# Optimization experiments

Measured on AMD Instinct MI355X. Metric: run time of the kernel, lower is better.

Reference implementation:

```python
import jax, jax.numpy as jnp
import numpy as np

N_NODES = 4096
IN_FEAT = 256
N_HEADS = 8
N_HIDDEN = 64  # out_features // n_heads
NEG_SLOPE = 0.2
EDGE_PROB = 0.05


def setup_inputs() -> dict:
    key = jax.random.key(0)
    k1, k2, k3, k4 = jax.random.split(key, 4)
    h = jax.random.normal(k1, (N_NODES, IN_FEAT), dtype=jnp.float32)
    # binary adjacency mask [N, N, 1] (broadcast over heads), as in the torch asserts
    adj_mat = (jax.random.uniform(k2, (N_NODES, N_NODES, 1)) < EDGE_PROB).astype(jnp.float32)
    # nn.Linear(in_features, n_heads*n_hidden, bias=False) weight: [H*F, in]
    W = jax.random.normal(k3, (N_HEADS * N_HIDDEN, IN_FEAT), dtype=jnp.float32) / np.sqrt(IN_FEAT)
    # nn.Linear(2*n_hidden, 1, bias=False) weight, flattened: [2*F]
    a = jax.random.normal(k4, (2 * N_HIDDEN,), dtype=jnp.float32) / np.sqrt(2 * N_HIDDEN)
    return {"h": h, "adj_mat": adj_mat, "W": W, "a": a}


def reference(h, adj_mat, W, a):
    n = h.shape[0]
    # g: [N, H, F]
    g = (h @ W.T).reshape(n, N_HEADS, N_HIDDEN)
    # attn(cat[g_i, g_j]) == a_l . g_i + a_r . g_j  (linear, no bias)
    a_l = a[:N_HIDDEN]
    a_r = a[N_HIDDEN:]
    el = jnp.einsum('ihf,f->ih', g, a_l)  # [N, H]
    er = jnp.einsum('jhf,f->jh', g, a_r)  # [N, H]
    e = jax.nn.leaky_relu(el[:, None, :] + er[None, :, :], NEG_SLOPE)  # [N, N, H]
    # note: original multiplies scores by adjacency (not masked_fill)
    e = e * adj_mat  # adj broadcasts over heads
    att = jax.nn.softmax(e, axis=1)  # softmax over source nodes j
    # dropout is identity at eval (dropout_rate=0.0)
    out = jnp.einsum('ijh,jhf->ihf', att, g)  # [N, H, F]
    return out.reshape(n, N_HEADS * N_HIDDEN)
```

## Files before the change

kernel.cpp:

```cpp
#include <hip/hip_runtime.h>

#define N_NODES 4096
#define IN_FEAT 256
#define N_HEADS 8
#define N_HIDDEN 64
#define OUT_FEAT (N_HEADS * N_HIDDEN)
#define NEG_SLOPE 0.2f

typedef _Float16 half8 __attribute__((ext_vector_type(8)));
typedef _Float16 h2 __attribute__((ext_vector_type(2)));
typedef float floatx4 __attribute__((ext_vector_type(4)));
typedef float f4 __attribute__((ext_vector_type(4)));

__global__ __launch_bounds__(256) void produce(
    const float* __restrict__ H, const float* __restrict__ adj,
    const float* __restrict__ Wt, const float* __restrict__ a,
    _Float16* __restrict__ GT16, float* __restrict__ elT,
    _Float16* __restrict__ eR1h, _Float16* __restrict__ eR2h,
    unsigned long long* __restrict__ bits) {
  __shared__ _Float16 SM[4 * 64 * 64];
  const int t = threadIdx.x;
  const int bx = blockIdx.x, by = blockIdx.y;

  if (by >= 8) {
    const int c = bx * 8 + (by - 8);
    const size_t W0 = (size_t)c * 512;
    const int wv = t >> 6, lane = t & 63;
    for (int k0 = 0; k0 < 128; k0 += 8) {
      float v[8];
#pragma unroll
      for (int k = 0; k < 8; ++k)
        v[k] = adj[(W0 + wv * 128 + k0 + k) * 64 + lane];
#pragma unroll
      for (int k = 0; k < 8; ++k) {
        unsigned long long m = __ballot(v[k] != 0.f);
        if (lane == 0) bits[W0 + wv * 128 + k0 + k] = m;
      }
    }
    return;
  }

  _Float16* Ah = SM;
  _Float16* Al = SM + 4096;
  _Float16* Bh = SM + 8192;
  _Float16* Bl = SM + 12288;
  const int w = t >> 6, l = t & 63;
  const int n16 = l & 15, q = l >> 4;
  const int bi = bx, bo = by;
  const int m0 = bi * 64 + w * 16;

  floatx4 acc[4];
#pragma unroll
  for (int ct = 0; ct < 4; ++ct) acc[ct] = (floatx4)0.f;

  for (int kc = 0; kc < 4; ++kc) {
    if (kc) __syncthreads();
#pragma unroll
    for (int p = 0; p < 4; ++p) {
      const int idx = p * 256 + t;
      const int r = idx >> 4;
      const int c4 = (idx & 15) << 2;
      const int dst = r * 64 + ((((idx & 15) >> 1)) ^ (r & 7)) * 8 + (idx & 1) * 4;
      float4 hv = *(const float4*)(H + (size_t)(bi * 64 + r) * IN_FEAT + kc * 64 + c4);
      float4 wv = *(const float4*)(Wt + (size_t)(bo * 64 + r) * IN_FEAT + kc * 64 + c4);
      union { _Float16 h[4]; int2 d; } hh_, hl_, wh_, wl_;
      hh_.h[0] = (_Float16)hv.x; hh_.h[1] = (_Float16)hv.y;
      hh_.h[2] = (_Float16)hv.z; hh_.h[3] = (_Float16)hv.w;
      hl_.h[0] = (_Float16)(hv.x - (float)hh_.h[0]);
      hl_.h[1] = (_Float16)(hv.y - (float)hh_.h[1]);
      hl_.h[2] = (_Float16)(hv.z - (float)hh_.h[2]);
      hl_.h[3] = (_Float16)(hv.w - (float)hh_.h[3]);
      wh_.h[0] = (_Float16)wv.x; wh_.h[1] = (_Float16)wv.y;
      wh_.h[2] = (_Float16)wv.z; wh_.h[3] = (_Float16)wv.w;
      wl_.h[0] = (_Float16)(wv.x - (float)wh_.h[0]);
      wl_.h[1] = (_Float16)(wv.y - (float)wh_.h[1]);
      wl_.h[2] = (_Float16)(wv.z - (float)wh_.h[2]);
      wl_.h[3] = (_Float16)(wv.w - (float)wh_.h[3]);
      *(int2*)&Ah[dst] = hh_.d;
      *(int2*)&Al[dst] = hl_.d;
      *(int2*)&Bh[dst] = wh_.d;
      *(int2*)&Bl[dst] = wl_.d;
    }
    __syncthreads();
#pragma unroll
    for (int ks = 0; ks < 2; ++ks) {
      const int ao = (w * 16 + n16) * 64 + (((ks << 2) + q) ^ (n16 & 7)) * 8;
      half8 Afh = *(const half8*)&Ah[ao];
      half8 Afl = *(const half8*)&Al[ao];
#pragma unroll
      for (int ct = 0; ct < 4; ++ct) {
        const int bofs = (ct * 16 + n16) * 64 + (((ks << 2) + q) ^ (n16 & 7)) * 8;
        half8 Bfh = *(const half8*)&Bh[bofs];
        half8 Bfl = *(const half8*)&Bl[bofs];
        acc[ct] = __builtin_amdgcn_mfma_f32_16x16x32_f16(Afh, Bfh, acc[ct], 0, 0, 0);
        acc[ct] = __builtin_amdgcn_mfma_f32_16x16x32_f16(Afl, Bfh, acc[ct], 0, 0, 0);
        acc[ct] = __builtin_amdgcn_mfma_f32_16x16x32_f16(Afh, Bfl, acc[ct], 0, 0, 0);
      }
    }
  }

  float aLv[4], aRv[4];
#pragma unroll
  for (int ct = 0; ct < 4; ++ct) {
    aLv[ct] = a[ct * 16 + n16];
    aRv[ct] = a[64 + ct * 16 + n16];
  }
#pragma unroll
  for (int reg = 0; reg < 4; ++reg) {
    float sl = 0.f, sr = 0.f;
#pragma unroll
    for (int ct = 0; ct < 4; ++ct) {
      sl = fmaf(acc[ct][reg], aLv[ct], sl);
      sr = fmaf(acc[ct][reg], aRv[ct], sr);
    }
#pragma unroll
    for (int off = 1; off < 16; off <<= 1) {
      sl += __shfl_xor(sl, off);
      sr += __shfl_xor(sr, off);
    }
    if (n16 == 0) {
      const int rowi = m0 + q * 4 + reg;
      elT[(size_t)bo * N_NODES + rowi] = sl;
      eR1h[(size_t)bo * N_NODES + rowi] = (_Float16)__expf(sr);
      eR2h[(size_t)bo * N_NODES + rowi] = (_Float16)__expf(0.2f * sr);
    }
  }

  __syncthreads();
  _Float16* LG = SM;
#pragma unroll
  for (int ct = 0; ct < 4; ++ct)
#pragma unroll
    for (int reg = 0; reg < 4; ++reg)
      LG[(w * 16 + q * 4 + reg) * 72 + ct * 16 + n16] = (_Float16)acc[ct][reg];
  __syncthreads();
  {
    const int f = t >> 2, jq = t & 3;
    union { _Float16 hh[16]; int4 v[2]; } u;
#pragma unroll
    for (int k = 0; k < 16; ++k) u.hh[k] = LG[(jq * 16 + k) * 72 + f];
    _Float16* dst = GT16 + (size_t)(bo * 64 + f) * N_NODES + bi * 64 + jq * 16;
    *(int4*)dst = u.v[0];
    *(int4*)(dst + 8) = u.v[1];
  }
}

__global__ __launch_bounds__(256) void attn_v12(
    const unsigned long long* __restrict__ bits, const _Float16* __restrict__ GT16,
    const float* __restrict__ elT, const _Float16* __restrict__ eR1h,
    const _Float16* __restrict__ eR2h, float* __restrict__ out) {
  __shared__ __align__(16) _Float16 Gt[2][2][2048];
  __shared__ __align__(16) _Float16 eRs1[2][2][32];
  __shared__ __align__(16) _Float16 eRs2[2][2][32];
  __shared__ float eL1s[32], eL2s[32];
  __shared__ float Zh1[32], Zfull[32];

  const int t = threadIdx.x;
  const int ib = blockIdx.x, h = blockIdx.y;
  const int i0 = ib * 32;
  const int w = t >> 6, l = t & 63, n16 = l & 15, q = l >> 4;
  const int rt = w & 1, jh = w >> 1;

  const _Float16* gsrcs[2];
  int ldsbase[2];
#pragma unroll
  for (int c = 0; c < 2; ++c) {
    const int flat = c * 256 + t;
    const int fjh = flat >> 8;
    const int ff = (flat >> 2) & 63;
    const int ss = flat & 3;
    const int cg = ss ^ ((ff >> 1) & 3);
    gsrcs[c] = GT16 + (size_t)(h * 64 + ff) * N_NODES + fjh * 2048 + cg * 8;
    ldsbase[c] = (c * 256 + w * 64) * 8;
  }
  const int era = t >> 3, ejh = (t >> 2) & 1, eseg = t & 3;
  const _Float16* esrc0 = (era ? eR2h : eR1h) + (size_t)h * N_NODES + ejh * 2048 + eseg * 8;
  const unsigned* bp = (const unsigned*)bits + (size_t)(i0 + rt * 16 + n16) * 128 + jh * 64;

  if (t < 32) {
    float e = elT[(size_t)h * N_NODES + i0 + t];
    eL1s[t] = __expf(e);
    eL2s[t] = __expf(0.2f * e);
  }
#pragma unroll
  for (int c = 0; c < 2; ++c)
    __builtin_amdgcn_global_load_lds(
        (const __attribute__((address_space(1))) unsigned int*)gsrcs[c],
        (__attribute__((address_space(3))) unsigned int*)(&Gt[0][0][0] + ldsbase[c]),
        16, 0, 0);
  if (t < 16) {
    int4 ev = *(const int4*)esrc0;
    *(int4*)&(era ? eRs2 : eRs1)[0][ejh][eseg * 8] = ev;
  }
  unsigned bvc = bp[0];
  __syncthreads();

  const _Float16 e1f = (_Float16)eL1s[rt * 16 + n16];
  const _Float16 e2f = (_Float16)eL2s[rt * 16 + n16];
  const h2 eL1h2 = {e1f, e1f};
  const h2 eL2h2 = {e2f, e2f};
  half8 Bones;
#pragma unroll
  for (int k = 0; k < 8; ++k) Bones[k] = (n16 == 0) ? (_Float16)1.f : (_Float16)0.f;

  floatx4 acc[4];
#pragma unroll
  for (int ft = 0; ft < 4; ++ft) acc[ft] = (floatx4)0.f;
  floatx4 acc5 = (floatx4)0.f;

  int par = 0;
  for (int step = 0; step < 64; ++step) {
    int4 ev;
    unsigned bvn = bvc;
    if (step + 1 < 64) {
      const int np = par ^ 1;
#pragma unroll
      for (int c = 0; c < 2; ++c)
        __builtin_amdgcn_global_load_lds(
            (const __attribute__((address_space(1))) unsigned int*)(gsrcs[c] + (step + 1) * 32),
            (__attribute__((address_space(3))) unsigned int*)(&Gt[np][0][0] + ldsbase[c]),
            16, 0, 0);
      if (t < 16) ev = *(const int4*)(esrc0 + (step + 1) * 32);
      bvn = bp[step + 1];
    }
    const _Float16* gt = &Gt[par][jh][0];
    {
      const unsigned byte = (bvc >> (q * 8)) & 0xffu;
      uint4 r1 = *(const uint4*)&eRs1[par][jh][q * 8];
      uint4 r2 = *(const uint4*)&eRs2[par][jh][q * 8];
      const unsigned r1a[4] = {r1.x, r1.y, r1.z, r1.w};
      const unsigned r2a[4] = {r2.x, r2.y, r2.z, r2.w};
      unsigned pr[4];
#pragma unroll
      for (int kk = 0; kk < 4; ++kk) {
        h2 pa = eL1h2 * __builtin_bit_cast(h2, r1a[kk]);
        h2 pb = eL2h2 * __builtin_bit_cast(h2, r2a[kk]);
        h2 pv = __builtin_elementwise_max(pa, pb);
        unsigned y = (byte >> (2 * kk)) & 3u;
        unsigned b01 = (y | (y << 15)) & 0x00010001u;
        unsigned keep = b01 * 0xffffu;
        pr[kk] = (__builtin_bit_cast(unsigned, pv) & keep) | (0x3C003C00u & ~keep);
      }
      const uint4 prv = {pr[0], pr[1], pr[2], pr[3]};
      half8 Af = __builtin_bit_cast(half8, prv);
#pragma unroll
      for (int ft = 0; ft < 4; ++ft) {
        half8 Bf = *(const half8*)&gt[(ft * 16 + n16) * 32 + ((q ^ ((n16 >> 1) & 3))) * 8];
        acc[ft] = __builtin_amdgcn_mfma_f32_16x16x32_f16(Af, Bf, acc[ft], 0, 0, 0);
      }
      acc5 = __builtin_amdgcn_mfma_f32_16x16x32_f16(Af, Bones, acc5, 0, 0, 0);
    }
    if (step + 1 < 64 && t < 16)
      *(int4*)&(era ? eRs2 : eRs1)[par ^ 1][ejh][eseg * 8] = ev;
    bvc = bvn;
    __syncthreads();
    par ^= 1;
  }

  float* comb = (float*)&Gt[0][0][0];
  if (jh == 1) {
#pragma unroll
    for (int ft = 0; ft < 4; ++ft)
#pragma unroll
      for (int reg = 0; reg < 4; ++reg)
        comb[(rt * 16 + q * 4 + reg) * 68 + ft * 16 + n16] = acc[ft][reg];
    if (n16 == 0) {
#pragma unroll
      for (int reg = 0; reg < 4; ++reg) Zh1[rt * 16 + q * 4 + reg] = acc5[reg];
    }
  }
  __syncthreads();
  if (jh == 0) {
#pragma unroll
    for (int ft = 0; ft < 4; ++ft)
#pragma unroll
      for (int reg = 0; reg < 4; ++reg)
        acc[ft][reg] += comb[(rt * 16 + q * 4 + reg) * 68 + ft * 16 + n16];
    if (n16 == 0) {
#pragma unroll
      for (int reg = 0; reg < 4; ++reg) {
        const int row = rt * 16 + q * 4 + reg;
        Zfull[row] = acc5[reg] + Zh1[row];
      }
    }
  }
  __syncthreads();
  if (jh == 0) {
#pragma unroll
    for (int reg = 0; reg < 4; ++reg) {
      const int row = rt * 16 + q * 4 + reg;
      const float invz = 1.f / Zfull[row];
      float* op = out + (size_t)(i0 + row) * OUT_FEAT + h * 64;
#pragma unroll
      for (int ft = 0; ft < 4; ++ft) op[ft * 16 + n16] = acc[ft][reg] * invz;
    }
  }
}

extern "C" void kernel_launch(void* const* d_in, const int* in_sizes, int n_in,
                              void* d_out, int out_size, void* d_ws, size_t ws_size,
                              hipStream_t stream) {
  const float* h   = (const float*)d_in[0];
  const float* adj = (const float*)d_in[1];
  const float* W   = (const float*)d_in[2];
  const float* a   = (const float*)d_in[3];
  float* out = (float*)d_out;

  char* ws = (char*)d_ws;
  _Float16* GT16 = (_Float16*)ws;
  unsigned long long* bits = (unsigned long long*)(ws + 4u * 1024 * 1024);
  float* elT = (float*)(ws + 6u * 1024 * 1024);
  _Float16* eR1h = (_Float16*)(ws + 6u * 1024 * 1024 + 128 * 1024);
  _Float16* eR2h = (_Float16*)(ws + 6u * 1024 * 1024 + 192 * 1024);

  produce<<<dim3(64, 16), 256, 0, stream>>>(h, adj, W, a, GT16, elT, eR1h, eR2h, bits);
  attn_v12<<<dim3(128, 8), 256, 0, stream>>>(bits, GT16, elT, eR1h, eR2h, out);
}
```

Baseline: 171.2 us.

## Split attention source dimension across two blocks and add combine kernel

Splits the attention kernel's loop over source nodes into two halves along a new grid z dimension, doubling the grid from 1024 to 2048 blocks, each doing 32 steps instead of 64. Partial numerators go to out or a workspace buffer, and partial normalizers go to Zp. A new combine kernel sums the halves and divides by Z. This targets low occupancy on a 256-CU device at the cost of an extra launch and extra global traffic for the partial outputs. It also raises launch bounds to hint at 8 blocks per CU.

```diff
diff --git a/kernel.cpp b/kernel.cpp
--- a/kernel.cpp
+++ b/kernel.cpp
@@ -145,10 +145,11 @@
   }
 }
 
-__global__ __launch_bounds__(256) void attn_v12(
+__global__ __launch_bounds__(256, 8) void attn_v13(
     const unsigned long long* __restrict__ bits, const _Float16* __restrict__ GT16,
     const float* __restrict__ elT, const _Float16* __restrict__ eR1h,
-    const _Float16* __restrict__ eR2h, float* __restrict__ out) {
+    const _Float16* __restrict__ eR2h, float* __restrict__ out,
+    float* __restrict__ O1, float* __restrict__ Zp) {
   __shared__ __align__(16) _Float16 Gt[2][2][2048];
   __shared__ __align__(16) _Float16 eRs1[2][2][32];
   __shared__ __align__(16) _Float16 eRs2[2][2][32];
@@ -156,7 +157,7 @@
   __shared__ float Zh1[32], Zfull[32];
 
   const int t = threadIdx.x;
-  const int ib = blockIdx.x, h = blockIdx.y;
+  const int ib = blockIdx.x, h = blockIdx.y, jz = blockIdx.z;
   const int i0 = ib * 32;
   const int w = t >> 6, l = t & 63, n16 = l & 15, q = l >> 4;
   const int rt = w & 1, jh = w >> 1;
@@ -170,12 +171,14 @@
     const int ff = (flat >> 2) & 63;
     const int ss = flat & 3;
     const int cg = ss ^ ((ff >> 1) & 3);
-    gsrcs[c] = GT16 + (size_t)(h * 64 + ff) * N_NODES + fjh * 2048 + cg * 8;
+    gsrcs[c] = GT16 + (size_t)(h * 64 + ff) * N_NODES + jz * 2048 + fjh * 1024 + cg * 8;
     ldsbase[c] = (c * 256 + w * 64) * 8;
   }
   const int era = t >> 3, ejh = (t >> 2) & 1, eseg = t & 3;
-  const _Float16* esrc0 = (era ? eR2h : eR1h) + (size_t)h * N_NODES + ejh * 2048 + eseg * 8;
-  const unsigned* bp = (const unsigned*)bits + (size_t)(i0 + rt * 16 + n16) * 128 + jh * 64;
+  const _Float16* esrc0 =
+      (era ? eR2h : eR1h) + (size_t)h * N_NODES + jz * 2048 + ejh * 1024 + eseg * 8;
+  const unsigned* bp =
+      (const unsigned*)bits + (size_t)(i0 + rt * 16 + n16) * 128 + jz * 64 + jh * 32;
 
   if (t < 32) {
     float e = elT[(size_t)h * N_NODES + i0 + t];
@@ -209,10 +212,10 @@
   floatx4 acc5 = (floatx4)0.f;
 
   int par = 0;
-  for (int step = 0; step < 64; ++step) {
+  for (int step = 0; step < 32; ++step) {
     int4 ev;
     unsigned bvn = bvc;
-    if (step + 1 < 64) {
+    if (step + 1 < 32) {
       const int np = par ^ 1;
 #pragma unroll
       for (int c = 0; c < 2; ++c)
@@ -250,7 +253,7 @@
       }
       acc5 = __builtin_amdgcn_mfma_f32_16x16x32_f16(Af, Bones, acc5, 0, 0, 0);
     }
-    if (step + 1 < 64 && t < 16)
+    if (step + 1 < 32 && t < 16)
       *(int4*)&(era ? eRs2 : eRs1)[par ^ 1][ejh][eseg * 8] = ev;
     bvc = bvn;
     __syncthreads();
@@ -285,16 +288,36 @@
     }
   }
   __syncthreads();
-  if (jh == 0) {
-#pragma unroll
-    for (int reg = 0; reg < 4; ++reg) {
-      const int row = rt * 16 + q * 4 + reg;
-      const float invz = 1.f / Zfull[row];
-      float* op = out + (size_t)(i0 + row) * OUT_FEAT + h * 64;
-#pragma unroll
-      for (int ft = 0; ft < 4; ++ft) op[ft * 16 + n16] = acc[ft][reg] * invz;
-    }
-  }
+  {
+    float* dst = (jz == 0) ? out : O1;
+    if (jh == 0) {
+#pragma unroll
+      for (int reg = 0; reg < 4; ++reg) {
+        const int row = rt * 16 + q * 4 + reg;
+        float* op = dst + (size_t)(i0 + row) * OUT_FEAT + h * 64;
+#pragma unroll
+        for (int ft = 0; ft < 4; ++ft) op[ft * 16 + n16] = acc[ft][reg];
+      }
+    }
+    if (t < 32) Zp[((size_t)(jz * 128 + ib) * 8 + h) * 32 + t] = Zfull[t];
+  }
+}
+
+__global__ __launch_bounds__(256) void combine(
+    const float* __restrict__ O1, const float* __restrict__ Zp,
+    float* __restrict__ out) {
+  const int t = threadIdx.x, ib = blockIdx.x, h = blockIdx.y;
+  const int row = t >> 3, f0 = (t & 7) * 8;
+  const size_t o = (size_t)(ib * 32 + row) * OUT_FEAT + h * 64 + f0;
+  f4 a0 = *(const f4*)(out + o);
+  f4 a1 = *(const f4*)(out + o + 4);
+  f4 b0 = *(const f4*)(O1 + o);
+  f4 b1 = *(const f4*)(O1 + o + 4);
+  const float Z = Zp[((size_t)ib * 8 + h) * 32 + row] +
+                  Zp[((size_t)(128 + ib) * 8 + h) * 32 + row];
+  const float invz = 1.f / Z;
+  *(f4*)(out + o) = (a0 + b0) * invz;
+  *(f4*)(out + o + 4) = (a1 + b1) * invz;
 }
 
 extern "C" void kernel_launch(void* const* d_in, const int* in_sizes, int n_in,
@@ -312,7 +335,10 @@
   float* elT = (float*)(ws + 6u * 1024 * 1024);
   _Float16* eR1h = (_Float16*)(ws + 6u * 1024 * 1024 + 128 * 1024);
   _Float16* eR2h = (_Float16*)(ws + 6u * 1024 * 1024 + 192 * 1024);
+  float* O1 = (float*)(ws + 8u * 1024 * 1024);
+  float* Zp = (float*)(ws + 16u * 1024 * 1024);
 
   produce<<<dim3(64, 16), 256, 0, stream>>>(h, adj, W, a, GT16, elT, eR1h, eR2h, bits);
-  attn_v12<<<dim3(128, 8), 256, 0, stream>>>(bits, GT16, elT, eR1h, eR2h, out);
+  attn_v13<<<dim3(128, 8, 2), 256, 0, stream>>>(bits, GT16, elT, eR1h, eR2h, out, O1, Zp);
+  combine<<<dim3(128, 8), 256, 0, stream>>>(O1, Zp, out);
 }
```

Result: slower. 175.9 us (+2.7%).
